# Kernel optimization log

Measured on AMD Instinct MI355X. Metric: run time of the kernel, lower is better.

## Reference

```python
import jax, jax.numpy as jnp
import numpy as np

TOP_K = 2
ROUTE_SCALE = 1.0
EPS = 1e-20

B, S, D = 2, 512, 1024
E = 8            # num_experts
F = 768          # moe_intermediate_size
FS = 768 * 1     # shared expert intermediate (moe_intermediate_size * num_shared_experts)


def setup_inputs() -> dict:
    key = jax.random.key(0)
    ks = jax.random.split(key, 9)
    s = 0.02
    return {
        "hidden_states": jax.random.normal(ks[0], (B, S, D), dtype=jnp.float32),
        "W_gate_router": jax.random.normal(ks[1], (D, E), dtype=jnp.float32) * s,
        "expert_bias": jnp.zeros((E,), dtype=jnp.float32),
        "Wg": jax.random.normal(ks[2], (E, D, F), dtype=jnp.float32) * s,
        "Wu": jax.random.normal(ks[3], (E, D, F), dtype=jnp.float32) * s,
        "Wd": jax.random.normal(ks[4], (E, F, D), dtype=jnp.float32) * s,
        "Wg_s": jax.random.normal(ks[5], (D, FS), dtype=jnp.float32) * s,
        "Wu_s": jax.random.normal(ks[6], (D, FS), dtype=jnp.float32) * s,
        "Wd_s": jax.random.normal(ks[7], (FS, D), dtype=jnp.float32) * s,
    }


def reference(hidden_states, W_gate_router, expert_bias, Wg, Wu, Wd, Wg_s, Wu_s, Wd_s):
    b, s, d = hidden_states.shape
    x = hidden_states.reshape(-1, d)                      # [T, D]
    T = x.shape[0]

    # ---- token-choice top-k router (sigmoid scoring, route_norm) ----
    logits = x @ W_gate_router                            # [T, E]
    scores = jax.nn.sigmoid(logits.astype(jnp.float32))   # [T, E] fp32
    _, sel = jax.lax.top_k(scores + expert_bias, TOP_K)   # [T, K] (bias only for selection)
    top_scores = jnp.take_along_axis(scores, sel, axis=1)  # [T, K]
    top_scores = top_scores / (top_scores.sum(-1, keepdims=True) + EPS)  # route_norm
    top_scores = top_scores * ROUTE_SCALE

    # ---- shared expert (always active) ----
    shared = (jax.nn.silu(x @ Wg_s) * (x @ Wu_s)) @ Wd_s  # [T, D]

    # ---- dispatch: N = T*K routed slots (scatter-add is order-independent,
    #      so the torch stable-argsort grouping is mathematically a no-op) ----
    tok = jnp.repeat(jnp.arange(T), TOP_K)                # [N] source token per slot
    exp = sel.reshape(-1)                                 # [N] expert per slot
    w = top_scores.reshape(-1)                            # [N]
    xr = x[tok]                                           # [N, D]

    # per-expert SiLU-GLU MLP, vectorized over experts then select own expert's row
    h = jax.nn.silu(jnp.einsum('nd,edf->enf', xr, Wg)) * jnp.einsum('nd,edf->enf', xr, Wu)
    out_all = jnp.einsum('enf,efd->end', h, Wd)           # [E, N, D]
    routed = out_all[exp, jnp.arange(exp.shape[0])]       # [N, D]
    routed = (routed.astype(jnp.float32) * w[:, None]).astype(hidden_states.dtype)

    # ---- combine: scatter-add routed outputs onto shared output ----
    out = shared.at[tok].add(routed)                      # [T, D]
    return out.reshape(b, s, d)
```

## Files before the change

kernel.cpp:

```cpp
#include <hip/hip_runtime.h>
#include <hip/hip_bf16.h>
#include <math.h>

#define T_TOK   1024
#define D_DIM   1024
#define E_NUM   8
#define F_DIM   768
#define N_SLOTS 2048

typedef unsigned short u16;
typedef unsigned int   u32;
typedef __attribute__((ext_vector_type(8))) short bf16x8;
typedef __attribute__((ext_vector_type(4))) float f32x4;

#define WS_SEL    0
#define WS_WTS    8192
#define WS_BUCKET 16384
#define WS_COUNTS 49152
#define WS_OFFS   49216
#define WS_POS    49280
#define WS_XB     65536
#define WS_H      (WS_XB + 2097152)
#define WS_Y      (WS_H + 4718592)

__device__ __forceinline__ u16 f2bf(float x) {
    u32 u = __float_as_uint(x);
    u += 0x7fffu + ((u >> 16) & 1u);
    return (u16)(u >> 16);
}
#define PKBF(hi, lo) __builtin_amdgcn_perm(__float_as_uint(hi), __float_as_uint(lo), 0x07060302u)

__device__ __forceinline__ void async16(const void* g, void* s) {
    __builtin_amdgcn_global_load_lds(
        (const __attribute__((address_space(1))) unsigned int*)g,
        (__attribute__((address_space(3))) unsigned int*)s, 16, 0, 0);
}

#define PIN()    __builtin_amdgcn_sched_barrier(0)
#define BAR()    do { PIN(); __builtin_amdgcn_s_barrier(); PIN(); } while (0)
#define WAITV(n) do { asm volatile("s_waitcnt vmcnt(" #n ")" ::: "memory"); PIN(); } while (0)
#define LGKM0()  do { asm volatile("s_waitcnt lgkmcnt(0)" ::: "memory"); PIN(); } while (0)

__global__ __launch_bounds__(256) void xrouter_kernel(
    const float* __restrict__ X, const float* __restrict__ Wr,
    const float* __restrict__ bias, u16* __restrict__ Xb,
    int* __restrict__ sel, float* __restrict__ wts)
{
    int t = blockIdx.x * 4 + (threadIdx.x >> 6);
    int lane = threadIdx.x & 63;
    const float* xrow = X + (size_t)t * D_DIM;
    u16* brow = Xb + (size_t)t * D_DIM;
    float acc[E_NUM];
#pragma unroll
    for (int e = 0; e < E_NUM; ++e) acc[e] = 0.f;
#pragma unroll
    for (int q = 0; q < 4; ++q) {
        int d = q * 256 + lane * 4;
        float4 v = *(const float4*)(xrow + d);
        ushort4 o;
        o.x = f2bf(v.x); o.y = f2bf(v.y); o.z = f2bf(v.z); o.w = f2bf(v.w);
        *(ushort4*)(brow + d) = o;
        const float xv[4] = {v.x, v.y, v.z, v.w};
#pragma unroll
        for (int jj = 0; jj < 4; ++jj) {
            const float4* wr = (const float4*)(Wr + (size_t)(d + jj) * E_NUM);
            float4 w0 = wr[0], w1 = wr[1];
            acc[0] += xv[jj] * w0.x; acc[1] += xv[jj] * w0.y;
            acc[2] += xv[jj] * w0.z; acc[3] += xv[jj] * w0.w;
            acc[4] += xv[jj] * w1.x; acc[5] += xv[jj] * w1.y;
            acc[6] += xv[jj] * w1.z; acc[7] += xv[jj] * w1.w;
        }
    }
#pragma unroll
    for (int e = 0; e < E_NUM; ++e)
#pragma unroll
        for (int off = 32; off > 0; off >>= 1)
            acc[e] += __shfl_xor(acc[e], off);
    if (lane == 0) {
        float s[E_NUM], b[E_NUM];
#pragma unroll
        for (int e = 0; e < E_NUM; ++e) {
            s[e] = 1.f / (1.f + expf(-acc[e]));
            b[e] = s[e] + bias[e];
        }
        int i1 = 0; float b1 = b[0];
#pragma unroll
        for (int e = 1; e < E_NUM; ++e) if (b[e] > b1) { b1 = b[e]; i1 = e; }
        int i2 = -1; float b2 = -INFINITY;
#pragma unroll
        for (int e = 0; e < E_NUM; ++e) {
            if (e == i1) continue;
            if (b[e] > b2) { b2 = b[e]; i2 = e; }
        }
        float s1 = s[i1], s2 = s[i2];
        float denom = s1 + s2 + 1e-20f;
        sel[2 * t] = i1; sel[2 * t + 1] = i2;
        wts[2 * t] = s1 / denom; wts[2 * t + 1] = s2 / denom;
    }
}

__global__ __launch_bounds__(512) void dispatch_kernel(
    const int* __restrict__ sel, int* __restrict__ bucket,
    int* __restrict__ counts, int* __restrict__ offs, int* __restrict__ pos)
{
    __shared__ int soffs[E_NUM + 1];
    int e = threadIdx.x >> 6;
    int lane = threadIdx.x & 63;
    int running = 0;
    for (int base = 0; base < N_SLOTS; base += 64) {
        int slot = base + lane;
        bool mine = (sel[slot] == e);
        unsigned long long mask = __ballot(mine);
        if (mine) {
            int rank = running + __popcll(mask & ((1ull << lane) - 1ull));
            bucket[e * T_TOK + rank] = slot;
        }
        running += __popcll(mask);
    }
    if (lane == 0) counts[e] = running;
    __syncthreads();
    if (threadIdx.x == 0) {
        int o = 0;
        for (int k = 0; k < E_NUM; ++k) { soffs[k] = o; offs[k] = o; o += counts[k]; }
        soffs[E_NUM] = o; offs[E_NUM] = o;
    }
    __syncthreads();
    int base_off = soffs[e];
    for (int r = lane; r < running; r += 64)
        pos[bucket[e * T_TOK + r]] = base_off + r;
}

__global__ __launch_bounds__(256, 2) void proj1(
    const u16* __restrict__ Xb,
    const float* __restrict__ Wg, const float* __restrict__ Wu,
    const float* __restrict__ Wgs, const float* __restrict__ Wus,
    u16* __restrict__ H,
    const int* __restrict__ bucket, const int* __restrict__ counts, const int* __restrict__ offs)
{
    const int i = blockIdx.x;
    const int cxcd = i & 7, m = i >> 3;
    const int y = m & 31, phi = m >> 5;
    const int panel = phi * 8 + cxcd;
    if (panel >= 108) return;
    const int unit = panel / 12, x = panel - unit * 12;

    int nrows, rbase; const float *Bg, *Bu;
    if (unit < E_NUM) {
        nrows = counts[unit]; rbase = offs[unit];
        Bg = Wg + (size_t)unit * D_DIM * F_DIM;
        Bu = Wu + (size_t)unit * D_DIM * F_DIM;
    } else { nrows = T_TOK; rbase = N_SLOTS; Bg = Wgs; Bu = Wus; }
    const int row0 = y * 64;
    if (row0 >= nrows) return;

    __shared__ u16 smem[3][6144];

    const int t = threadIdx.x;
    const int wv = t >> 6, lane = t & 63, l15 = lane & 15;
    const int wm = wv >> 1, wn = wv & 1;

    int arow = 16 * wv + (lane >> 2);
    int grow = min(row0 + arow, nrows - 1);
    if (unit < E_NUM) grow = bucket[unit * T_TOK + grow] >> 1;
    const int fA = ((lane >> 2) & 3) ^ ((lane >> 4) & 1);
    const u16* srcA = Xb + (size_t)grow * D_DIM + ((lane & 3) ^ fA) * 8;

    const int ngrp = t & 31, kgrp = t >> 5;
    const int n0 = 4 * ngrp, k0 = 4 * kgrp;
    const float* srcB = ((n0 < 64) ? Bg : Bu) + (size_t)k0 * F_DIM + x * 64 + (n0 & 63);
    const int wch  = (kgrp >> 1) ^ (ngrp & 3);
    const int woff = 2048 + n0 * 32 + wch * 8 + (kgrp & 1) * 4;

    const int g4  = lane >> 4;
    const int chA = g4 ^ (l15 & 3) ^ ((l15 >> 2) & 1);
    const int chB = g4 ^ ((l15 >> 2) & 3);
    int offA[2], offG[2], offU[2];
#pragma unroll
    for (int ri = 0; ri < 2; ++ri)
        offA[ri] = (wm * 32 + ri * 16 + l15) * 32 + chA * 8;
#pragma unroll
    for (int ci = 0; ci < 2; ++ci) {
        offG[ci] = 2048 + (wn * 32 + ci * 16 + l15) * 32 + chB * 8;
        offU[ci] = offG[ci] + 64 * 32;
    }

    f32x4 accg[2][2], accu[2][2];
    const f32x4 z4 = {0.f, 0.f, 0.f, 0.f};
#pragma unroll
    for (int ri = 0; ri < 2; ++ri)
#pragma unroll
        for (int ci = 0; ci < 2; ++ci) { accg[ri][ci] = z4; accu[ri][ci] = z4; }

    float4 SA[4], SB[4];
#define LOADB1(SV, tile) do { \
    const float* _s = srcB + (size_t)((tile) * 32) * F_DIM; \
    SV[0] = *(const float4*)(_s);             _s += F_DIM; \
    SV[1] = *(const float4*)(_s);             _s += F_DIM; \
    SV[2] = *(const float4*)(_s);             _s += F_DIM; \
    SV[3] = *(const float4*)(_s); } while (0)
#define WRITEB1(SV, buf) do { \
    u16* _bb = smem[(buf)]; \
    const float* _f0 = (const float*)&SV[0]; const float* _f1 = (const float*)&SV[1]; \
    const float* _f2 = (const float*)&SV[2]; const float* _f3 = (const float*)&SV[3]; \
    _Pragma("unroll") \
    for (int j = 0; j < 4; ++j) { \
        u32 _w0 = PKBF(_f1[j], _f0[j]); \
        u32 _w1 = PKBF(_f3[j], _f2[j]); \
        *(uint2*)&_bb[woff + j * 32] = make_uint2(_w0, _w1); \
    } } while (0)
#define COMP1(buf) do { \
    const u16* _p = smem[(buf)]; \
    bf16x8 _av[2], _bg[2], _bu[2]; \
    _Pragma("unroll") for (int ri = 0; ri < 2; ++ri) _av[ri] = *(const bf16x8*)&_p[offA[ri]]; \
    _Pragma("unroll") for (int ci = 0; ci < 2; ++ci) { \
        _bg[ci] = *(const bf16x8*)&_p[offG[ci]]; \
        _bu[ci] = *(const bf16x8*)&_p[offU[ci]]; } \
    _Pragma("unroll") for (int ri = 0; ri < 2; ++ri) \
        _Pragma("unroll") for (int ci = 0; ci < 2; ++ci) { \
            accg[ri][ci] = __builtin_amdgcn_mfma_f32_16x16x32_bf16(_av[ri], _bg[ci], accg[ri][ci], 0, 0, 0); \
            accu[ri][ci] = __builtin_amdgcn_mfma_f32_16x16x32_bf16(_av[ri], _bu[ci], accu[ri][ci], 0, 0, 0); } \
    } while (0)
#define BODY1(tt, SV) do { \
    WAITV(6); \
    WRITEB1(SV, ((tt) + 2) % 3); \
    LOADB1(SV, min((tt) + 4, 31)); \
    LGKM0(); \
    BAR(); \
    COMP1((tt) % 3); \
    BAR(); \
    async16(srcA + min((tt) + 3, 31) * 32, &smem[(tt) % 3][wv * 512]); \
} while (0)

    LOADB1(SA, 0);
    LOADB1(SB, 1);
    WAITV(4);
    WRITEB1(SA, 0);
    async16(srcA, &smem[0][wv * 512]);
    LOADB1(SA, 2);
    WAITV(5);
    WRITEB1(SB, 1);
    async16(srcA + 32, &smem[1][wv * 512]);
    LOADB1(SB, 3);
    async16(srcA + 64, &smem[2][wv * 512]);

    for (int tt = 0; tt < 32; tt += 2) {
        BODY1(tt, SA);
        BODY1(tt + 1, SB);
    }
#undef BODY1
#undef COMP1
#undef WRITEB1
#undef LOADB1

    const int lg = lane >> 4;
#pragma unroll
    for (int ri = 0; ri < 2; ++ri)
#pragma unroll
        for (int ci = 0; ci < 2; ++ci) {
            int n = x * 64 + wn * 32 + ci * 16 + l15;
#pragma unroll
            for (int r = 0; r < 4; ++r) {
                int row = row0 + wm * 32 + ri * 16 + lg * 4 + r;
                if (row >= nrows) continue;
                float gv = accg[ri][ci][r];
                float uv = accu[ri][ci][r];
                H[(size_t)(rbase + row) * F_DIM + n] =
                    f2bf(gv / (1.f + __expf(-gv)) * uv);
            }
        }
}

__global__ __launch_bounds__(256, 2) void proj2(
    const u16* __restrict__ H,
    const float* __restrict__ Wd, const float* __restrict__ Wds,
    float* __restrict__ Y,
    const int* __restrict__ counts, const int* __restrict__ offs)
{
    const int i = blockIdx.x;
    const int cxcd = i & 7, m = i >> 3;
    const int y = m & 31, phi = m >> 5;
    const int panel = phi * 8 + cxcd;
    const int unit = panel >> 4, x = panel & 15;

    int nrows, rbase; const float* Bm;
    if (unit < E_NUM) {
        nrows = counts[unit]; rbase = offs[unit];
        Bm = Wd + (size_t)unit * F_DIM * D_DIM;
    } else { nrows = T_TOK; rbase = N_SLOTS; Bm = Wds; }
    const int row0 = y * 64;
    if (row0 >= nrows) return;

    __shared__ u16 smem[3][4096];

    const int t = threadIdx.x;
    const int wv = t >> 6, lane = t & 63, l15 = lane & 15;
    const int wm = wv >> 1, wn = wv & 1;

    int arow = 16 * wv + (lane >> 2);
    int grow = rbase + min(row0 + arow, nrows - 1);
    const int fA = ((lane >> 2) & 3) ^ ((lane >> 4) & 1);
    const u16* srcA = H + (size_t)grow * F_DIM + ((lane & 3) ^ fA) * 8;

    const int ngrp = t & 15, kgrp = t >> 4;
    const int n0 = 4 * ngrp, k0 = 2 * kgrp;
    const float* srcB = Bm + (size_t)k0 * D_DIM + x * 64 + n0;
    const int wch  = (k0 >> 3) ^ (ngrp & 3);
    const int woff = 2048 + n0 * 32 + wch * 8 + (k0 & 7);

    const int g4  = lane >> 4;
    const int chA = g4 ^ (l15 & 3) ^ ((l15 >> 2) & 1);
    const int chB = g4 ^ ((l15 >> 2) & 3);
    int offA[2], offB[2];
#pragma unroll
    for (int ri = 0; ri < 2; ++ri)
        offA[ri] = (wm * 32 + ri * 16 + l15) * 32 + chA * 8;
#pragma unroll
    for (int ci = 0; ci < 2; ++ci)
        offB[ci] = 2048 + (wn * 32 + ci * 16 + l15) * 32 + chB * 8;

    f32x4 acc[2][2];
    const f32x4 z4 = {0.f, 0.f, 0.f, 0.f};
#pragma unroll
    for (int ri = 0; ri < 2; ++ri)
#pragma unroll
        for (int ci = 0; ci < 2; ++ci) acc[ri][ci] = z4;

    float4 SA[2], SB[2];
#define LOADB2(SV, tile) do { \
    const float* _s = srcB + (size_t)((tile) * 32) * D_DIM; \
    SV[0] = *(const float4*)(_s); \
    SV[1] = *(const float4*)(_s + D_DIM); } while (0)
#define WRITEB2(SV, buf) do { \
    u16* _bb = smem[(buf)]; \
    const float* _f0 = (const float*)&SV[0]; const float* _f1 = (const float*)&SV[1]; \
    _Pragma("unroll") \
    for (int j = 0; j < 4; ++j) { \
        u32 _w = PKBF(_f1[j], _f0[j]); \
        *(u32*)&_bb[woff + j * 32] = _w; \
    } } while (0)
#define COMP2(buf) do { \
    const u16* _p = smem[(buf)]; \
    bf16x8 _av[2], _bv[2]; \
    _Pragma("unroll") for (int ri = 0; ri < 2; ++ri) _av[ri] = *(const bf16x8*)&_p[offA[ri]]; \
    _Pragma("unroll") for (int ci = 0; ci < 2; ++ci) _bv[ci] = *(const bf16x8*)&_p[offB[ci]]; \
    _Pragma("unroll") for (int ri = 0; ri < 2; ++ri) \
        _Pragma("unroll") for (int ci = 0; ci < 2; ++ci) \
            acc[ri][ci] = __builtin_amdgcn_mfma_f32_16x16x32_bf16(_av[ri], _bv[ci], acc[ri][ci], 0, 0, 0); \
    } while (0)
#define BODY2(tt, SV) do { \
    WAITV(4); \
    WRITEB2(SV, ((tt) + 2) % 3); \
    LOADB2(SV, min((tt) + 4, 23)); \
    LGKM0(); \
    BAR(); \
    COMP2((tt) % 3); \
    BAR(); \
    async16(srcA + min((tt) + 3, 23) * 32, &smem[(tt) % 3][wv * 512]); \
} while (0)

    LOADB2(SA, 0);
    LOADB2(SB, 1);
    WAITV(2);
    WRITEB2(SA, 0);
    async16(srcA, &smem[0][wv * 512]);
    LOADB2(SA, 2);
    WAITV(3);
    WRITEB2(SB, 1);
    async16(srcA + 32, &smem[1][wv * 512]);
    LOADB2(SB, 3);
    async16(srcA + 64, &smem[2][wv * 512]);

    for (int tt = 0; tt < 24; tt += 2) {
        BODY2(tt, SA);
        BODY2(tt + 1, SB);
    }
#undef BODY2
#undef COMP2
#undef WRITEB2
#undef LOADB2

    const int lg = lane >> 4;
#pragma unroll
    for (int ri = 0; ri < 2; ++ri)
#pragma unroll
        for (int ci = 0; ci < 2; ++ci) {
            int n = x * 64 + wn * 32 + ci * 16 + l15;
#pragma unroll
            for (int r = 0; r < 4; ++r) {
                int row = row0 + wm * 32 + ri * 16 + lg * 4 + r;
                if (row >= nrows) continue;
                Y[(size_t)(rbase + row) * D_DIM + n] = acc[ri][ci][r];
            }
        }
}

__global__ __launch_bounds__(256) void combine_kernel(
    const float* __restrict__ Y, const int* __restrict__ pos,
    const float* __restrict__ wts, float* __restrict__ out)
{
    int t = blockIdx.x;
    int d = threadIdx.x * 4;
    int p0 = pos[2 * t], p1 = pos[2 * t + 1];
    float w0 = wts[2 * t], w1 = wts[2 * t + 1];
    float4 a = *(const float4*)(Y + (size_t)(N_SLOTS + t) * D_DIM + d);
    float4 b = *(const float4*)(Y + (size_t)p0 * D_DIM + d);
    float4 cc = *(const float4*)(Y + (size_t)p1 * D_DIM + d);
    float4 o;
    o.x = a.x + w0 * b.x + w1 * cc.x;
    o.y = a.y + w0 * b.y + w1 * cc.y;
    o.z = a.z + w0 * b.z + w1 * cc.z;
    o.w = a.w + w0 * b.w + w1 * cc.w;
    *(float4*)(out + (size_t)t * D_DIM + d) = o;
}

extern "C" void kernel_launch(void* const* d_in, const int* in_sizes, int n_in,
                              void* d_out, int out_size, void* d_ws, size_t ws_size,
                              hipStream_t stream) {
    const float* X    = (const float*)d_in[0];
    const float* Wr   = (const float*)d_in[1];
    const float* bias = (const float*)d_in[2];
    const float* Wg   = (const float*)d_in[3];
    const float* Wu   = (const float*)d_in[4];
    const float* Wd   = (const float*)d_in[5];
    const float* Wgs  = (const float*)d_in[6];
    const float* Wus  = (const float*)d_in[7];
    const float* Wds  = (const float*)d_in[8];
    float* out = (float*)d_out;

    char* ws = (char*)d_ws;
    int*   sel    = (int*)(ws + WS_SEL);
    float* wtsv   = (float*)(ws + WS_WTS);
    int*   bucket = (int*)(ws + WS_BUCKET);
    int*   counts = (int*)(ws + WS_COUNTS);
    int*   offs   = (int*)(ws + WS_OFFS);
    int*   pos    = (int*)(ws + WS_POS);
    u16*   Xb     = (u16*)(ws + WS_XB);
    u16*   H      = (u16*)(ws + WS_H);
    float* Y      = (float*)(ws + WS_Y);

    xrouter_kernel<<<256, 256, 0, stream>>>(X, Wr, bias, Xb, sel, wtsv);
    dispatch_kernel<<<1, 512, 0, stream>>>(sel, bucket, counts, offs, pos);

    proj1<<<3584, 256, 0, stream>>>(Xb, Wg, Wu, Wgs, Wus, H, bucket, counts, offs);
    proj2<<<4608, 256, 0, stream>>>(H, Wd, Wds, Y, counts, offs);
    combine_kernel<<<T_TOK, 256, 0, stream>>>(Y, pos, wtsv, out);
}
```

Measured before the change: 99.83 us.

## Restructure MoE GEMM pipelines to double-buffered 64-wide K tiles with register staging

Result: faster. 85.23 us (-14.6%).

```diff
diff --git a/kernel.cpp b/kernel.cpp
--- a/kernel.cpp
+++ b/kernel.cpp
@@ -29,17 +29,6 @@
     return (u16)(u >> 16);
 }
 #define PKBF(hi, lo) __builtin_amdgcn_perm(__float_as_uint(hi), __float_as_uint(lo), 0x07060302u)
-
-__device__ __forceinline__ void async16(const void* g, void* s) {
-    __builtin_amdgcn_global_load_lds(
-        (const __attribute__((address_space(1))) unsigned int*)g,
-        (__attribute__((address_space(3))) unsigned int*)s, 16, 0, 0);
-}
-
-#define PIN()    __builtin_amdgcn_sched_barrier(0)
-#define BAR()    do { PIN(); __builtin_amdgcn_s_barrier(); PIN(); } while (0)
-#define WAITV(n) do { asm volatile("s_waitcnt vmcnt(" #n ")" ::: "memory"); PIN(); } while (0)
-#define LGKM0()  do { asm volatile("s_waitcnt lgkmcnt(0)" ::: "memory"); PIN(); } while (0)
 
 __global__ __launch_bounds__(256) void xrouter_kernel(
     const float* __restrict__ X, const float* __restrict__ Wr,
@@ -130,7 +119,7 @@
         pos[bucket[e * T_TOK + r]] = base_off + r;
 }
 
-__global__ __launch_bounds__(256, 2) void proj1(
+__global__ __launch_bounds__(256, 3) void proj1(
     const u16* __restrict__ Xb,
     const float* __restrict__ Wg, const float* __restrict__ Wu,
     const float* __restrict__ Wgs, const float* __restrict__ Wus,
@@ -153,36 +142,26 @@
     const int row0 = y * 64;
     if (row0 >= nrows) return;
 
-    __shared__ u16 smem[3][6144];
+    __shared__ u16 smem[2][192 * 64];
 
     const int t = threadIdx.x;
-    const int wv = t >> 6, lane = t & 63, l15 = lane & 15;
+    const int wv = t >> 6, lane = t & 63, l15 = lane & 15, g = lane >> 4;
     const int wm = wv >> 1, wn = wv & 1;
 
-    int arow = 16 * wv + (lane >> 2);
-    int grow = min(row0 + arow, nrows - 1);
+    const int ar = t >> 2, ac = t & 3;
+    int grow = min(row0 + ar, nrows - 1);
     if (unit < E_NUM) grow = bucket[unit * T_TOK + grow] >> 1;
-    const int fA = ((lane >> 2) & 3) ^ ((lane >> 4) & 1);
-    const u16* srcA = Xb + (size_t)grow * D_DIM + ((lane & 3) ^ fA) * 8;
-
-    const int ngrp = t & 31, kgrp = t >> 5;
-    const int n0 = 4 * ngrp, k0 = 4 * kgrp;
-    const float* srcB = ((n0 < 64) ? Bg : Bu) + (size_t)k0 * F_DIM + x * 64 + (n0 & 63);
-    const int wch  = (kgrp >> 1) ^ (ngrp & 3);
-    const int woff = 2048 + n0 * 32 + wch * 8 + (kgrp & 1) * 4;
-
-    const int g4  = lane >> 4;
-    const int chA = g4 ^ (l15 & 3) ^ ((l15 >> 2) & 1);
-    const int chB = g4 ^ ((l15 >> 2) & 3);
-    int offA[2], offG[2], offU[2];
-#pragma unroll
-    for (int ri = 0; ri < 2; ++ri)
-        offA[ri] = (wm * 32 + ri * 16 + l15) * 32 + chA * 8;
-#pragma unroll
-    for (int ci = 0; ci < 2; ++ci) {
-        offG[ci] = 2048 + (wn * 32 + ci * 16 + l15) * 32 + chB * 8;
-        offU[ci] = offG[ci] + 64 * 32;
-    }
+    const u16* srcA = Xb + (size_t)grow * D_DIM + ac * 8;
+    const int wA0 = ar * 64 + ((ac     ^ (ar & 7)) * 8);
+    const int wA1 = ar * 64 + (((ac+4) ^ (ar & 7)) * 8);
+
+    const int bn = (t & 63) | (((t >> 6) & 1) << 6);
+    const int bh = t >> 7;
+    const float* srcB = ((bn < 64) ? Bg : Bu) + (size_t)(bh * 32) * F_DIM + x * 64 + (bn & 63);
+    int wB[4];
+#pragma unroll
+    for (int q = 0; q < 4; ++q)
+        wB[q] = (64 + bn) * 64 + (((bh * 4 + q) ^ (bn & 7)) * 8);
 
     f32x4 accg[2][2], accu[2][2];
     const f32x4 z4 = {0.f, 0.f, 0.f, 0.f};
@@ -191,68 +170,61 @@
 #pragma unroll
         for (int ci = 0; ci < 2; ++ci) { accg[ri][ci] = z4; accu[ri][ci] = z4; }
 
-    float4 SA[4], SB[4];
-#define LOADB1(SV, tile) do { \
-    const float* _s = srcB + (size_t)((tile) * 32) * F_DIM; \
-    SV[0] = *(const float4*)(_s);             _s += F_DIM; \
-    SV[1] = *(const float4*)(_s);             _s += F_DIM; \
-    SV[2] = *(const float4*)(_s);             _s += F_DIM; \
-    SV[3] = *(const float4*)(_s); } while (0)
-#define WRITEB1(SV, buf) do { \
-    u16* _bb = smem[(buf)]; \
-    const float* _f0 = (const float*)&SV[0]; const float* _f1 = (const float*)&SV[1]; \
-    const float* _f2 = (const float*)&SV[2]; const float* _f3 = (const float*)&SV[3]; \
-    _Pragma("unroll") \
-    for (int j = 0; j < 4; ++j) { \
-        u32 _w0 = PKBF(_f1[j], _f0[j]); \
-        u32 _w1 = PKBF(_f3[j], _f2[j]); \
-        *(uint2*)&_bb[woff + j * 32] = make_uint2(_w0, _w1); \
-    } } while (0)
+    uint4 pa0, pa1;
+    float pb[32];
+#define LOAD1(kt) do { \
+    pa0 = *(const uint4*)(srcA + (kt)); \
+    pa1 = *(const uint4*)(srcA + (kt) + 32); \
+    const float* _bp = srcB + (size_t)(kt) * F_DIM; \
+    _Pragma("unroll") \
+    for (int ii = 0; ii < 32; ++ii) pb[ii] = _bp[(size_t)ii * F_DIM]; \
+} while (0)
+#define WRITE1(buf) do { \
+    *(uint4*)&smem[buf][wA0] = pa0; \
+    *(uint4*)&smem[buf][wA1] = pa1; \
+    _Pragma("unroll") \
+    for (int q = 0; q < 4; ++q) { \
+        u32 pk[4]; \
+        _Pragma("unroll") \
+        for (int j = 0; j < 4; ++j) pk[j] = PKBF(pb[8*q + 2*j + 1], pb[8*q + 2*j]); \
+        *(uint4*)&smem[buf][wB[q]] = *(const uint4*)pk; \
+    } \
+} while (0)
 #define COMP1(buf) do { \
-    const u16* _p = smem[(buf)]; \
-    bf16x8 _av[2], _bg[2], _bu[2]; \
-    _Pragma("unroll") for (int ri = 0; ri < 2; ++ri) _av[ri] = *(const bf16x8*)&_p[offA[ri]]; \
-    _Pragma("unroll") for (int ci = 0; ci < 2; ++ci) { \
-        _bg[ci] = *(const bf16x8*)&_p[offG[ci]]; \
-        _bu[ci] = *(const bf16x8*)&_p[offU[ci]]; } \
-    _Pragma("unroll") for (int ri = 0; ri < 2; ++ri) \
-        _Pragma("unroll") for (int ci = 0; ci < 2; ++ci) { \
-            accg[ri][ci] = __builtin_amdgcn_mfma_f32_16x16x32_bf16(_av[ri], _bg[ci], accg[ri][ci], 0, 0, 0); \
-            accu[ri][ci] = __builtin_amdgcn_mfma_f32_16x16x32_bf16(_av[ri], _bu[ci], accu[ri][ci], 0, 0, 0); } \
-    } while (0)
-#define BODY1(tt, SV) do { \
-    WAITV(6); \
-    WRITEB1(SV, ((tt) + 2) % 3); \
-    LOADB1(SV, min((tt) + 4, 31)); \
-    LGKM0(); \
-    BAR(); \
-    COMP1((tt) % 3); \
-    BAR(); \
-    async16(srcA + min((tt) + 3, 31) * 32, &smem[(tt) % 3][wv * 512]); \
-} while (0)
-
-    LOADB1(SA, 0);
-    LOADB1(SB, 1);
-    WAITV(4);
-    WRITEB1(SA, 0);
-    async16(srcA, &smem[0][wv * 512]);
-    LOADB1(SA, 2);
-    WAITV(5);
-    WRITEB1(SB, 1);
-    async16(srcA + 32, &smem[1][wv * 512]);
-    LOADB1(SB, 3);
-    async16(srcA + 64, &smem[2][wv * 512]);
-
-    for (int tt = 0; tt < 32; tt += 2) {
-        BODY1(tt, SA);
-        BODY1(tt + 1, SB);
-    }
-#undef BODY1
+    const u16* _p = smem[buf]; \
+    _Pragma("unroll") \
+    for (int kk = 0; kk < 2; ++kk) { \
+        const int ch = (((kk << 2) | g) ^ (l15 & 7)) * 8; \
+        bf16x8 _a[2], _bg[2], _bu[2]; \
+        _Pragma("unroll") \
+        for (int ri = 0; ri < 2; ++ri) \
+            _a[ri] = *(const bf16x8*)&_p[(wm * 32 + ri * 16 + l15) * 64 + ch]; \
+        _Pragma("unroll") \
+        for (int ci = 0; ci < 2; ++ci) { \
+            _bg[ci] = *(const bf16x8*)&_p[(64  + wn * 32 + ci * 16 + l15) * 64 + ch]; \
+            _bu[ci] = *(const bf16x8*)&_p[(128 + wn * 32 + ci * 16 + l15) * 64 + ch]; \
+        } \
+        _Pragma("unroll") \
+        for (int ri = 0; ri < 2; ++ri) \
+            _Pragma("unroll") \
+            for (int ci = 0; ci < 2; ++ci) { \
+                accg[ri][ci] = __builtin_amdgcn_mfma_f32_16x16x32_bf16(_a[ri], _bg[ci], accg[ri][ci], 0, 0, 0); \
+                accu[ri][ci] = __builtin_amdgcn_mfma_f32_16x16x32_bf16(_a[ri], _bu[ci], accu[ri][ci], 0, 0, 0); \
+            } \
+    } \
+} while (0)
+
+    LOAD1(0);
+    for (int tt = 0; tt < 16; ++tt) {
+        WRITE1(tt & 1);
+        if (tt + 1 < 16) LOAD1((tt + 1) * 64);
+        __syncthreads();
+        COMP1(tt & 1);
+    }
+#undef LOAD1
+#undef WRITE1
 #undef COMP1
-#undef WRITEB1
-#undef LOADB1
-
-    const int lg = lane >> 4;
+
 #pragma unroll
     for (int ri = 0; ri < 2; ++ri)
 #pragma unroll
@@ -260,7 +232,7 @@
             int n = x * 64 + wn * 32 + ci * 16 + l15;
 #pragma unroll
             for (int r = 0; r < 4; ++r) {
-                int row = row0 + wm * 32 + ri * 16 + lg * 4 + r;
+                int row = row0 + wm * 32 + ri * 16 + g * 4 + r;
                 if (row >= nrows) continue;
                 float gv = accg[ri][ci][r];
                 float uv = accu[ri][ci][r];
@@ -270,7 +242,7 @@
         }
 }
 
-__global__ __launch_bounds__(256, 2) void proj2(
+__global__ __launch_bounds__(256, 3) void proj2(
     const u16* __restrict__ H,
     const float* __restrict__ Wd, const float* __restrict__ Wds,
     float* __restrict__ Y,
@@ -290,33 +262,25 @@
     const int row0 = y * 64;
     if (row0 >= nrows) return;
 
-    __shared__ u16 smem[3][4096];
+    __shared__ u16 smem[2][128 * 64];
 
     const int t = threadIdx.x;
-    const int wv = t >> 6, lane = t & 63, l15 = lane & 15;
+    const int wv = t >> 6, lane = t & 63, l15 = lane & 15, g = lane >> 4;
     const int wm = wv >> 1, wn = wv & 1;
 
-    int arow = 16 * wv + (lane >> 2);
-    int grow = rbase + min(row0 + arow, nrows - 1);
-    const int fA = ((lane >> 2) & 3) ^ ((lane >> 4) & 1);
-    const u16* srcA = H + (size_t)grow * F_DIM + ((lane & 3) ^ fA) * 8;
-
-    const int ngrp = t & 15, kgrp = t >> 4;
-    const int n0 = 4 * ngrp, k0 = 2 * kgrp;
-    const float* srcB = Bm + (size_t)k0 * D_DIM + x * 64 + n0;
-    const int wch  = (k0 >> 3) ^ (ngrp & 3);
-    const int woff = 2048 + n0 * 32 + wch * 8 + (k0 & 7);
-
-    const int g4  = lane >> 4;
-    const int chA = g4 ^ (l15 & 3) ^ ((l15 >> 2) & 1);
-    const int chB = g4 ^ ((l15 >> 2) & 3);
-    int offA[2], offB[2];
-#pragma unroll
-    for (int ri = 0; ri < 2; ++ri)
-        offA[ri] = (wm * 32 + ri * 16 + l15) * 32 + chA * 8;
-#pragma unroll
-    for (int ci = 0; ci < 2; ++ci)
-        offB[ci] = 2048 + (wn * 32 + ci * 16 + l15) * 32 + chB * 8;
+    const int ar = t >> 2, ac = t & 3;
+    const int grow = rbase + min(row0 + ar, nrows - 1);
+    const u16* srcA = H + (size_t)grow * F_DIM + ac * 8;
+    const int wA0 = ar * 64 + ((ac     ^ (ar & 7)) * 8);
+    const int wA1 = ar * 64 + (((ac+4) ^ (ar & 7)) * 8);
+
+    const int bn = t & 63;
+    const int bq = t >> 6;
+    const float* srcB = Bm + (size_t)(bq * 16) * D_DIM + x * 64 + bn;
+    int wB[2];
+#pragma unroll
+    for (int q = 0; q < 2; ++q)
+        wB[q] = (64 + bn) * 64 + (((bq * 2 + q) ^ (bn & 7)) * 8);
 
     f32x4 acc[2][2];
     const f32x4 z4 = {0.f, 0.f, 0.f, 0.f};
@@ -325,61 +289,57 @@
 #pragma unroll
         for (int ci = 0; ci < 2; ++ci) acc[ri][ci] = z4;
 
-    float4 SA[2], SB[2];
-#define LOADB2(SV, tile) do { \
-    const float* _s = srcB + (size_t)((tile) * 32) * D_DIM; \
-    SV[0] = *(const float4*)(_s); \
-    SV[1] = *(const float4*)(_s + D_DIM); } while (0)
-#define WRITEB2(SV, buf) do { \
-    u16* _bb = smem[(buf)]; \
-    const float* _f0 = (const float*)&SV[0]; const float* _f1 = (const float*)&SV[1]; \
-    _Pragma("unroll") \
-    for (int j = 0; j < 4; ++j) { \
-        u32 _w = PKBF(_f1[j], _f0[j]); \
-        *(u32*)&_bb[woff + j * 32] = _w; \
-    } } while (0)
+    uint4 pa0, pa1;
+    float pb[16];
+#define LOAD2(kt) do { \
+    pa0 = *(const uint4*)(srcA + (kt)); \
+    pa1 = *(const uint4*)(srcA + (kt) + 32); \
+    const float* _bp = srcB + (size_t)(kt) * D_DIM; \
+    _Pragma("unroll") \
+    for (int ii = 0; ii < 16; ++ii) pb[ii] = _bp[(size_t)ii * D_DIM]; \
+} while (0)
+#define WRITE2(buf) do { \
+    *(uint4*)&smem[buf][wA0] = pa0; \
+    *(uint4*)&smem[buf][wA1] = pa1; \
+    _Pragma("unroll") \
+    for (int q = 0; q < 2; ++q) { \
+        u32 pk[4]; \
+        _Pragma("unroll") \
+        for (int j = 0; j < 4; ++j) pk[j] = PKBF(pb[8*q + 2*j + 1], pb[8*q + 2*j]); \
+        *(uint4*)&smem[buf][wB[q]] = *(const uint4*)pk; \
+    } \
+} while (0)
 #define COMP2(buf) do { \
-    const u16* _p = smem[(buf)]; \
-    bf16x8 _av[2], _bv[2]; \
-    _Pragma("unroll") for (int ri = 0; ri < 2; ++ri) _av[ri] = *(const bf16x8*)&_p[offA[ri]]; \
-    _Pragma("unroll") for (int ci = 0; ci < 2; ++ci) _bv[ci] = *(const bf16x8*)&_p[offB[ci]]; \
-    _Pragma("unroll") for (int ri = 0; ri < 2; ++ri) \
-        _Pragma("unroll") for (int ci = 0; ci < 2; ++ci) \
-            acc[ri][ci] = __builtin_amdgcn_mfma_f32_16x16x32_bf16(_av[ri], _bv[ci], acc[ri][ci], 0, 0, 0); \
-    } while (0)
-#define BODY2(tt, SV) do { \
-    WAITV(4); \
-    WRITEB2(SV, ((tt) + 2) % 3); \
-    LOADB2(SV, min((tt) + 4, 23)); \
-    LGKM0(); \
-    BAR(); \
-    COMP2((tt) % 3); \
-    BAR(); \
-    async16(srcA + min((tt) + 3, 23) * 32, &smem[(tt) % 3][wv * 512]); \
-} while (0)
-
-    LOADB2(SA, 0);
-    LOADB2(SB, 1);
-    WAITV(2);
-    WRITEB2(SA, 0);
-    async16(srcA, &smem[0][wv * 512]);
-    LOADB2(SA, 2);
-    WAITV(3);
-    WRITEB2(SB, 1);
-    async16(srcA + 32, &smem[1][wv * 512]);
-    LOADB2(SB, 3);
-    async16(srcA + 64, &smem[2][wv * 512]);
-
-    for (int tt = 0; tt < 24; tt += 2) {
-        BODY2(tt, SA);
-        BODY2(tt + 1, SB);
-    }
-#undef BODY2
+    const u16* _p = smem[buf]; \
+    _Pragma("unroll") \
+    for (int kk = 0; kk < 2; ++kk) { \
+        const int ch = (((kk << 2) | g) ^ (l15 & 7)) * 8; \
+        bf16x8 _a[2], _b[2]; \
+        _Pragma("unroll") \
+        for (int ri = 0; ri < 2; ++ri) \
+            _a[ri] = *(const bf16x8*)&_p[(wm * 32 + ri * 16 + l15) * 64 + ch]; \
+        _Pragma("unroll") \
+        for (int ci = 0; ci < 2; ++ci) \
+            _b[ci] = *(const bf16x8*)&_p[(64 + wn * 32 + ci * 16 + l15) * 64 + ch]; \
+        _Pragma("unroll") \
+        for (int ri = 0; ri < 2; ++ri) \
+            _Pragma("unroll") \
+            for (int ci = 0; ci < 2; ++ci) \
+                acc[ri][ci] = __builtin_amdgcn_mfma_f32_16x16x32_bf16(_a[ri], _b[ci], acc[ri][ci], 0, 0, 0); \
+    } \
+} while (0)
+
+    LOAD2(0);
+    for (int tt = 0; tt < 12; ++tt) {
+        WRITE2(tt & 1);
+        if (tt + 1 < 12) LOAD2((tt + 1) * 64);
+        __syncthreads();
+        COMP2(tt & 1);
+    }
+#undef LOAD2
+#undef WRITE2
 #undef COMP2
-#undef WRITEB2
-#undef LOADB2
-
-    const int lg = lane >> 4;
+
 #pragma unroll
     for (int ri = 0; ri < 2; ++ri)
 #pragma unroll
@@ -387,7 +347,7 @@
             int n = x * 64 + wn * 32 + ci * 16 + l15;
 #pragma unroll
             for (int r = 0; r < 4; ++r) {
-                int row = row0 + wm * 32 + ri * 16 + lg * 4 + r;
+                int row = row0 + wm * 32 + ri * 16 + g * 4 + r;
                 if (row >= nrows) continue;
                 Y[(size_t)(rbase + row) * D_DIM + n] = acc[ri][ci][r];
             }
```
